# Kernel tuning notes

Measured on AMD Instinct MI355X. Metric: run time of the kernel, lower is better.

The kernel has to match this reference:

```python
import itertools
import jax, jax.numpy as jnp
import numpy as np

N_OBJECTS = 32
GRAPHLET_SIZE = 3
N_FILTERS = 16
REL_DIM = 16
BATCH = 32
N_GROUP_QUERIES = 512
BETA = 1.0

# static combinatorial groups: all C(32,3) = 4960 index triples
GROUP_IDX = jnp.asarray(
    np.array(list(itertools.combinations(range(N_OBJECTS), GRAPHLET_SIZE)), dtype=np.int32)
)  # (G, g)


def setup_inputs() -> dict:
    key = jax.random.key(0)
    k1, k2, k3 = jax.random.split(key, 3)
    inputs = jax.random.normal(k1, (BATCH, N_OBJECTS, N_OBJECTS, REL_DIM), dtype=jnp.float32)
    group_logits = jax.random.normal(k2, (N_GROUP_QUERIES, N_OBJECTS), dtype=jnp.float32)
    filters = jax.random.normal(k3, (N_FILTERS, GRAPHLET_SIZE, GRAPHLET_SIZE, REL_DIM), dtype=jnp.float32)
    return {"inputs": inputs, "group_logits": group_logits, "filters": filters}


def reference(inputs, group_logits, filters):
    idx = GROUP_IDX  # (G, g)
    # gather sub-relation tensors for every group in one fused advanced-index:
    # (B, G, g, g, D)
    sub_rel = inputs[:, idx[:, :, None], idx[:, None, :], :]
    # relational inner product with all filters: (B, G, F)
    rel_conv = jnp.einsum('bgijd,fijd->bgf', sub_rel, filters)
    # soft group weights
    sp = jax.nn.softplus(group_logits)            # (Gi, N)
    group_obj_w = sp[:, idx]                      # (Gi, G, g) -- gather along object axis
    group_w = jnp.prod(group_obj_w, axis=-1)      # (Gi, G)
    norm_w = jax.nn.softmax(BETA * group_w, axis=-1)  # (Gi, G)
    # contract over combinatorial groups: (B, Gi, F)
    out = jnp.einsum('bnr,gn->bgr', rel_conv, norm_w)
    return out
```

## Files before the change

kernel.cpp:

```cpp
#include <hip/hip_runtime.h>
#include <hip/hip_bf16.h>

#define N_OBJ   32
#define G_TOTAL 4960
#define GPAD    5120
#define N_FILT  16
#define REL_D   16
#define BATCH   32
#define NQ      512
#define KWAVE   1280
#define NIT     40

typedef __attribute__((ext_vector_type(8))) short bf16x8;
typedef __attribute__((ext_vector_type(4))) float f32x4;

static __device__ inline unsigned short f2bf(float x) {
    union { float f; unsigned int u; } v; v.f = x;
    unsigned int r = v.u + 0x7fffu + ((v.u >> 16) & 1u);
    return (unsigned short)(r >> 16);
}
static __device__ inline float bfbits2f(unsigned int bits) {
    union { unsigned int u; float f; } v; v.u = bits; return v.f;
}
static __device__ inline void gload_lds16(const void* g, void* l) {
    __builtin_amdgcn_global_load_lds(
        (const __attribute__((address_space(1))) unsigned int*)g,
        (__attribute__((address_space(3))) unsigned int*)(unsigned int)(uintptr_t)l,
        16, 0, 0);
}
static __device__ inline void unrank3(int g, int& a, int& b, int& c) {
    int rem = g;
    for (a = 0; a < 30; a++) { int cnt = ((31 - a) * (30 - a)) >> 1; if (rem < cnt) break; rem -= cnt; }
    for (b = a + 1; b < 31; b++) { if (rem < 31 - b) break; rem -= 31 - b; }
    c = b + 1 + rem;
}

__global__ __launch_bounds__(256) void k_front(const float* __restrict__ logits,
                                               const float* __restrict__ inputs,
                                               const float* __restrict__ filters,
                                               unsigned short* __restrict__ normw,
                                               unsigned short* __restrict__ D) {
    __shared__ __align__(16) char smem[11648];
    int t = threadIdx.x;
    int role = blockIdx.x;

    if (role < NQ) {
        float* sp  = (float*)smem;
        float* red = (float*)(smem + 128);
        unsigned short* wrow = (unsigned short*)(smem + 144);
        int q = role;
        if (t < N_OBJ) {
            float x = logits[q * N_OBJ + t];
            sp[t] = (x > 15.f) ? x : log1pf(expf(x));
        }
        if (t < GPAD - G_TOTAL) wrow[G_TOTAL + t] = 0;
        __syncthreads();

        int g0 = t * 20;
        int aa, bb, cc;
        unrank3(g0, aa, bb, cc);

        float w[20];
        float lmax = -1e30f;
#pragma unroll
        for (int k = 0; k < 20; k++) {
            float v = -1e30f;
            if (g0 + k < G_TOTAL) v = sp[aa] * sp[bb] * sp[cc];
            w[k] = v;
            lmax = fmaxf(lmax, v);
            cc++;
            if (cc >= 32) { bb++; cc = bb + 1; if (cc >= 32) { aa++; bb = aa + 1; cc = bb + 1; } }
        }
#pragma unroll
        for (int off = 32; off; off >>= 1) lmax = fmaxf(lmax, __shfl_down(lmax, off, 64));
        if ((t & 63) == 0) red[t >> 6] = lmax;
        __syncthreads();
        float wmax = fmaxf(fmaxf(red[0], red[1]), fmaxf(red[2], red[3]));

        float lsum = 0.f;
#pragma unroll
        for (int k = 0; k < 20; k++) {
            float e = (g0 + k < G_TOTAL) ? expf(w[k] - wmax) : 0.f;
            w[k] = e;
            lsum += e;
        }
#pragma unroll
        for (int off = 32; off; off >>= 1) lsum += __shfl_down(lsum, off, 64);
        __syncthreads();
        if ((t & 63) == 0) red[t >> 6] = lsum;
        __syncthreads();
        float inv = 1.f / (red[0] + red[1] + red[2] + red[3]);

#pragma unroll
        for (int k = 0; k < 20; k++)
            if (g0 + k < G_TOTAL) wrow[g0 + k] = f2bf(w[k] * inv);
        __syncthreads();
        uint4* dstrow = (uint4*)(normw + (size_t)q * GPAD);
        const uint4* srow = (const uint4*)wrow;
        for (int i = t; i < 640; i += 256) dstrow[i] = srow[i];
    } else {
        float* flt = (float*)smem;
        int bid = role - NQ;
        int p = bid >> 7;
        int xb = bid & 127;
        for (int i = t; i < 576; i += 256) {
            int i4 = i * 4;
            int f = i4 / 144;
            int r = i4 - f * 144;
            *(float4*)&flt[f * 180 + (r >> 4) * 20 + (r & 15)] = *(const float4*)(filters + i4);
        }
        __syncthreads();

        int row = xb * 256 + t;
        int b = row >> 10, xy = row & 1023;
        const float4* src = (const float4*)(inputs + (size_t)row * 16);
        float4 s0 = src[0], s1 = src[1], s2 = src[2], s3 = src[3];

        unsigned short outv[16];
        const float* fb = &flt[p * 20];
#pragma unroll
        for (int f = 0; f < 16; f++) {
            float4 f0 = *(const float4*)(fb + f * 180);
            float4 f1 = *(const float4*)(fb + f * 180 + 4);
            float4 f2 = *(const float4*)(fb + f * 180 + 8);
            float4 f3 = *(const float4*)(fb + f * 180 + 12);
            float d = s0.x * f0.x + s0.y * f0.y + s0.z * f0.z + s0.w * f0.w;
            d += s1.x * f1.x + s1.y * f1.y + s1.z * f1.z + s1.w * f1.w;
            d += s2.x * f2.x + s2.y * f2.y + s2.z * f2.z + s2.w * f2.w;
            d += s3.x * f3.x + s3.y * f3.y + s3.z * f3.z + s3.w * f3.w;
            outv[f] = f2bf(d);
        }
        uint4* dst = (uint4*)(D + ((size_t)(xy * 9 + p)) * 512 + b * 16);
        dst[0] = ((uint4*)outv)[0];
        dst[1] = ((uint4*)outv)[1];
    }
}

__global__ __launch_bounds__(256) void k_mid(const unsigned short* __restrict__ D,
                                             unsigned short* __restrict__ relT) {
    __shared__ int tri[8];
    int t = threadIdx.x;
    int g0 = blockIdx.x * 8;
    if (t < 8) {
        int a, b, c;
        unrank3(g0 + t, a, b, c);
        tri[t] = a | (b << 8) | (c << 16);
    }
    __syncthreads();

    float s0[8], s1[8];
#pragma unroll
    for (int g = 0; g < 8; g++) {
        int pk = tri[g];
        int xs[3] = { pk & 255, (pk >> 8) & 255, (pk >> 16) & 255 };
        float x0 = 0.f, x1 = 0.f;
#pragma unroll
        for (int i = 0; i < 3; i++)
#pragma unroll
            for (int j = 0; j < 3; j++) {
                int xy = xs[i] * 32 + xs[j];
                unsigned int v = *(const unsigned int*)(D + (size_t)(xy * 9 + i * 3 + j) * 512 + t * 2);
                x0 += bfbits2f(v << 16);
                x1 += bfbits2f(v & 0xffff0000u);
            }
        s0[g] = x0; s1[g] = x1;
    }
    unsigned int pack0[4], pack1[4];
#pragma unroll
    for (int k = 0; k < 4; k++) {
        pack0[k] = f2bf(s0[2 * k]) | ((unsigned int)f2bf(s0[2 * k + 1]) << 16);
        pack1[k] = f2bf(s1[2 * k]) | ((unsigned int)f2bf(s1[2 * k + 1]) << 16);
    }
    *(uint4*)(relT + (size_t)(2 * t) * GPAD + g0)     = *(uint4*)pack0;
    *(uint4*)(relT + (size_t)(2 * t + 1) * GPAD + g0) = *(uint4*)pack1;
}

__global__ __launch_bounds__(256) void k_gemmf(const unsigned short* __restrict__ A,
                                               const unsigned short* __restrict__ Bm,
                                               float* __restrict__ out) {
    __shared__ __align__(16) char smem[32768];
    int tid = threadIdx.x;
    int wave = tid >> 6, lane = tid & 63;
    int q0 = blockIdx.x * 32, n0 = blockIdx.y * 32;
    int row16 = lane & 15, quad = lane >> 4;

    int srow = lane >> 2;
    int schunk = (lane & 3) ^ ((srow >> 1) & 3);
    const unsigned short* gA = A  + (size_t)(q0 + srow) * GPAD + wave * KWAVE + schunk * 8;
    const unsigned short* gB = Bm + (size_t)(n0 + srow) * GPAD + wave * KWAVE + schunk * 8;
    char* lw = smem + wave * 8192;
    char* ld = lw + lane * 16;

    f32x4 acc[2][2] = {};
    int fslot = (quad ^ ((row16 >> 1) & 3)) * 16;

    gload_lds16(gA,             ld);
    gload_lds16(gA + 16 * GPAD, ld + 1024);
    gload_lds16(gB,             ld + 2048);
    gload_lds16(gB + 16 * GPAD, ld + 3072);

#pragma unroll 2
    for (int it = 0; it < NIT; ++it) {
        int buf = it & 1;
        asm volatile("s_waitcnt vmcnt(0)" ::: "memory");
        const char* fb = lw + buf * 4096;
        bf16x8 a0 = *(const bf16x8*)(fb + row16 * 64 + fslot);
        bf16x8 a1 = *(const bf16x8*)(fb + 1024 + row16 * 64 + fslot);
        bf16x8 b0 = *(const bf16x8*)(fb + 2048 + row16 * 64 + fslot);
        bf16x8 b1 = *(const bf16x8*)(fb + 3072 + row16 * 64 + fslot);
        asm volatile("s_waitcnt lgkmcnt(0)" ::: "memory");
        if (it + 1 < NIT) {
            int ko = (it + 1) * 32;
            char* ln = ld + (buf ^ 1) * 4096;
            gload_lds16(gA + ko,             ln);
            gload_lds16(gA + 16 * GPAD + ko, ln + 1024);
            gload_lds16(gB + ko,             ln + 2048);
            gload_lds16(gB + 16 * GPAD + ko, ln + 3072);
        }
        acc[0][0] = __builtin_amdgcn_mfma_f32_16x16x32_bf16(a0, b0, acc[0][0], 0, 0, 0);
        acc[0][1] = __builtin_amdgcn_mfma_f32_16x16x32_bf16(a0, b1, acc[0][1], 0, 0, 0);
        acc[1][0] = __builtin_amdgcn_mfma_f32_16x16x32_bf16(a1, b0, acc[1][0], 0, 0, 0);
        acc[1][1] = __builtin_amdgcn_mfma_f32_16x16x32_bf16(a1, b1, acc[1][1], 0, 0, 0);
    }

    __syncthreads();
    float* red = (float*)smem;
#pragma unroll
    for (int mi = 0; mi < 2; mi++)
#pragma unroll
        for (int ni = 0; ni < 2; ni++)
#pragma unroll
            for (int r = 0; r < 4; r++)
                red[wave * 1024 + (mi * 16 + quad * 4 + r) * 32 + ni * 16 + row16] =
                    acc[mi][ni][r];
    __syncthreads();

    int e = tid * 4;
    float4 s = *(const float4*)&red[e];
#pragma unroll
    for (int w = 1; w < 4; w++) {
        float4 v = *(const float4*)&red[w * 1024 + e];
        s.x += v.x; s.y += v.y; s.z += v.z; s.w += v.w;
    }
    int ql = e >> 5, nl = e & 31;
    int nn = n0 + nl;
    *(float4*)(out + (size_t)(nn >> 4) * (NQ * REL_D) + (q0 + ql) * 16 + (nn & 15)) = s;
}

extern "C" void kernel_launch(void* const* d_in, const int* in_sizes, int n_in,
                              void* d_out, int out_size, void* d_ws, size_t ws_size,
                              hipStream_t stream) {
    const float* inputs  = (const float*)d_in[0];
    const float* logits  = (const float*)d_in[1];
    const float* filters = (const float*)d_in[2];
    float* out = (float*)d_out;

    char* ws = (char*)d_ws;
    unsigned short* normw = (unsigned short*)ws;
    unsigned short* D     = (unsigned short*)(ws + 5242880);
    unsigned short* relT  = (unsigned short*)(ws + 14680064);

    k_front<<<NQ + 1152, 256, 0, stream>>>(logits, inputs, filters, normw, D);
    k_mid<<<G_TOTAL / 8, 256, 0, stream>>>(D, relT);
    k_gemmf<<<dim3(16, 16), 256, 0, stream>>>(normw, relT, out);
}
```

Before: 97.62 us.

## Deepen GEMM prefetch to two stages and remap blocks for XCD locality

The final GEMM kernel now issues global-to-LDS loads two iterations ahead, waiting with vmcnt(4) instead of draining every load before each step. This is meant to hide more global memory latency per wave. The grid also becomes a flat 1D launch whose block index is remapped so that blocks on the same XCD share Q and N tiles, aiming for better L2 reuse. This adds a peeled last iteration, and the buffer being refilled is the one just read, which depends on the lgkmcnt wait coming before the new loads are issued.

```diff
diff --git a/kernel.cpp b/kernel.cpp
--- a/kernel.cpp
+++ b/kernel.cpp
@@ -181,7 +181,11 @@
     __shared__ __align__(16) char smem[32768];
     int tid = threadIdx.x;
     int wave = tid >> 6, lane = tid & 63;
-    int q0 = blockIdx.x * 32, n0 = blockIdx.y * 32;
+    int blk = blockIdx.x;
+    int xcd = blk & 7, loc = blk >> 3;
+    int qt = (xcd & 3) * 4 + (loc & 3);
+    int nt = (xcd >> 2) * 8 + (loc >> 2);
+    int q0 = qt * 32, n0 = nt * 32;
     int row16 = lane & 15, quad = lane >> 4;
 
     int srow = lane >> 2;
@@ -194,34 +198,48 @@
     f32x4 acc[2][2] = {};
     int fslot = (quad ^ ((row16 >> 1) & 3)) * 16;
 
-    gload_lds16(gA,             ld);
-    gload_lds16(gA + 16 * GPAD, ld + 1024);
-    gload_lds16(gB,             ld + 2048);
-    gload_lds16(gB + 16 * GPAD, ld + 3072);
-
+#define GSTAGE(itn, bufsel)                                   \
+    {                                                         \
+        char* dd_ = ld + (bufsel) * 4096;                     \
+        int ko_ = (itn) * 32;                                 \
+        gload_lds16(gA + ko_,             dd_);               \
+        gload_lds16(gA + 16 * GPAD + ko_, dd_ + 1024);        \
+        gload_lds16(gB + ko_,             dd_ + 2048);        \
+        gload_lds16(gB + 16 * GPAD + ko_, dd_ + 3072);        \
+    }
+
+    GSTAGE(0, 0)
+    GSTAGE(1, 1)
 #pragma unroll 2
-    for (int it = 0; it < NIT; ++it) {
+    for (int it = 0; it < NIT - 1; ++it) {
         int buf = it & 1;
+        asm volatile("s_waitcnt vmcnt(4)" ::: "memory");
+        const char* fb = lw + buf * 4096;
+        bf16x8 a0 = *(const bf16x8*)(fb + row16 * 64 + fslot);
+        bf16x8 a1 = *(const bf16x8*)(fb + 1024 + row16 * 64 + fslot);
+        bf16x8 b0 = *(const bf16x8*)(fb + 2048 + row16 * 64 + fslot);
+        bf16x8 b1 = *(const bf16x8*)(fb + 3072 + row16 * 64 + fslot);
+        asm volatile("s_waitcnt lgkmcnt(0)" ::: "memory");
+        if (it + 2 < NIT) GSTAGE(it + 2, buf)
+        acc[0][0] = __builtin_amdgcn_mfma_f32_16x16x32_bf16(a0, b0, acc[0][0], 0, 0, 0);
+        acc[0][1] = __builtin_amdgcn_mfma_f32_16x16x32_bf16(a0, b1, acc[0][1], 0, 0, 0);
+        acc[1][0] = __builtin_amdgcn_mfma_f32_16x16x32_bf16(a1, b0, acc[1][0], 0, 0, 0);
+        acc[1][1] = __builtin_amdgcn_mfma_f32_16x16x32_bf16(a1, b1, acc[1][1], 0, 0, 0);
+    }
+    {
+        int buf = (NIT - 1) & 1;
         asm volatile("s_waitcnt vmcnt(0)" ::: "memory");
         const char* fb = lw + buf * 4096;
         bf16x8 a0 = *(const bf16x8*)(fb + row16 * 64 + fslot);
         bf16x8 a1 = *(const bf16x8*)(fb + 1024 + row16 * 64 + fslot);
         bf16x8 b0 = *(const bf16x8*)(fb + 2048 + row16 * 64 + fslot);
         bf16x8 b1 = *(const bf16x8*)(fb + 3072 + row16 * 64 + fslot);
-        asm volatile("s_waitcnt lgkmcnt(0)" ::: "memory");
-        if (it + 1 < NIT) {
-            int ko = (it + 1) * 32;
-            char* ln = ld + (buf ^ 1) * 4096;
-            gload_lds16(gA + ko,             ln);
-            gload_lds16(gA + 16 * GPAD + ko, ln + 1024);
-            gload_lds16(gB + ko,             ln + 2048);
-            gload_lds16(gB + 16 * GPAD + ko, ln + 3072);
-        }
         acc[0][0] = __builtin_amdgcn_mfma_f32_16x16x32_bf16(a0, b0, acc[0][0], 0, 0, 0);
         acc[0][1] = __builtin_amdgcn_mfma_f32_16x16x32_bf16(a0, b1, acc[0][1], 0, 0, 0);
         acc[1][0] = __builtin_amdgcn_mfma_f32_16x16x32_bf16(a1, b0, acc[1][0], 0, 0, 0);
         acc[1][1] = __builtin_amdgcn_mfma_f32_16x16x32_bf16(a1, b1, acc[1][1], 0, 0, 0);
     }
+#undef GSTAGE
 
     __syncthreads();
     float* red = (float*)smem;
@@ -262,5 +280,5 @@
 
     k_front<<<NQ + 1152, 256, 0, stream>>>(logits, inputs, filters, normw, D);
     k_mid<<<G_TOTAL / 8, 256, 0, stream>>>(D, relT);
-    k_gemmf<<<dim3(16, 16), 256, 0, stream>>>(normw, relT, out);
-}
+    k_gemmf<<<dim3(256), 256, 0, stream>>>(normw, relT, out);
+}
```

Result: no change. 96.94 us (-0.7%).
